# Performance work log

Measured on AMD Instinct MI355X. Metric: run time of the kernel, lower is better.

Reference implementation:

```python
import jax, jax.numpy as jnp
import numpy as np

B, D, H, W_ = 2, 256, 64, 64


def setup_inputs() -> dict:
    key = jax.random.key(0)
    k1, k2 = jax.random.split(key)
    x = jax.random.normal(k1, (B, D, H, W_), dtype=jnp.float32)
    W = jax.random.normal(k2, (3 * D, D), dtype=jnp.float32) * 0.02  # 1x1 conv weight [out,in]
    b = jnp.zeros((3 * D,), dtype=jnp.float32)
    return {"x": x, "W": W, "b": b}


def reference(x, W, b):
    Bs, d, h, w = x.shape
    N = h * w
    sqrtV = d ** 0.25  # sqrt(sqrt(d)); q,k each divided -> qk^T / sqrt(d)
    # 1x1 conv == per-pixel linear over channels
    qkv = jnp.einsum('bchw,oc->bohw', x, W) + b[None, :, None, None]
    q, k, v = jnp.split(qkv, 3, axis=1)
    q = q.reshape(Bs, d, N).transpose(0, 2, 1) / sqrtV  # [B,N,d]
    k = k.reshape(Bs, d, N).transpose(0, 2, 1) / sqrtV
    v = v.reshape(Bs, d, N).transpose(0, 2, 1)
    # Sinkhorn (eps=1, max_iter=1, uniform marginals 1/N), log domain.
    # cost C = -q k^T  =>  -C = q k^T (softmax-style logits)
    negC = jnp.einsum('bnd,bmd->bnm', q, k)  # [B,N,N]
    logm = jnp.log(1.0 / N + 1e-8).astype(x.dtype)
    u = logm - jax.nn.logsumexp(negC, axis=-1)            # [B,N] row update
    vpot = logm - jax.nn.logsumexp(negC + u[..., None], axis=-2)  # [B,N] col update
    pi = jnp.exp(negC + u[..., None] + vpot[:, None, :])  # transport plan = attn
    out = jnp.einsum('bnm,bmd->bnd', pi, v)               # [B,N,d]
    return out.transpose(0, 2, 1).reshape(Bs, d, h, w)
```

## Files before the change

### kernel.cpp

```cpp
#include <hip/hip_runtime.h>
#include <hip/hip_bf16.h>
#include <math.h>

typedef __bf16 bf16;
typedef __bf16 bf16x8 __attribute__((ext_vector_type(8)));
typedef __bf16 bf16x4 __attribute__((ext_vector_type(4)));
typedef float floatx4 __attribute__((ext_vector_type(4)));

typedef const __attribute__((address_space(1))) void* gas_t;
typedef __attribute__((address_space(3))) void* las_t;

#define NPIX 4096
#define DCH 256

#define OFF_XB   ((size_t)0)
#define OFF_WB   ((size_t)4194304)
#define OFF_Q    ((size_t)4587520)
#define OFF_K    ((size_t)8781824)
#define OFF_V    ((size_t)12976128)
#define OFF_E    ((size_t)17170432)
#define OFF_VPP  ((size_t)84279296)
#define OFF_RP   ((size_t)88473600)
#define OFF_CP   ((size_t)89522176)
#define OFF_PART ((size_t)90570752)

__device__ __forceinline__ void stage_tile(const bf16* __restrict__ g0, size_t rstride,
                                           bf16* lds, int t) {
  const int wbase = (t >> 6) << 6;
#pragma unroll
  for (int i = 0; i < 4; i++) {
    int slot = i * 256 + t;
    int row = slot >> 3, seg = slot & 7;
    const bf16* g = g0 + (size_t)row * rstride + ((seg ^ (row & 7)) << 3);
    bf16* l = lds + (size_t)(i * 256 + wbase) * 8;
    __builtin_amdgcn_global_load_lds((gas_t)g, (las_t)l, 16, 0, 0);
  }
}

__global__ __launch_bounds__(256) void prep(
    const float* __restrict__ x, const float* __restrict__ W,
    bf16* __restrict__ xb, bf16* __restrict__ wb)
{
  const int t = threadIdx.x;
  if (blockIdx.y == 4) {
    int gid = (blockIdx.z * 64 + blockIdx.x) * 256 + t;
    for (int i = gid; i < 49152; i += 32768) {
      float4 v = *(const float4*)(W + (size_t)i * 4);
      bf16x4 pk = { (bf16)v.x, (bf16)v.y, (bf16)v.z, (bf16)v.w };
      *(bf16x4*)(wb + (size_t)i * 4) = pk;
    }
    return;
  }
  __shared__ float ts[64][65];
  const int b = blockIdx.z, n0 = blockIdx.x * 64, c0 = blockIdx.y * 64;
  const float* xp = x + ((size_t)b * DCH + c0) * NPIX + n0;
  for (int i = 0; i < 4; i++) {
    int slot = t + i * 256;
    int c = slot >> 4, nq = (slot & 15) * 4;
    float4 v = *(const float4*)(xp + (size_t)c * NPIX + nq);
    ts[c][nq + 0] = v.x; ts[c][nq + 1] = v.y; ts[c][nq + 2] = v.z; ts[c][nq + 3] = v.w;
  }
  __syncthreads();
  for (int i = 0; i < 2; i++) {
    int slot = t + i * 256;
    int n = slot >> 3, cq = (slot & 7) * 8;
    bf16x8 pk;
    for (int j = 0; j < 8; j++) pk[j] = (bf16)ts[cq + j][n];
    *(bf16x8*)(xb + ((size_t)b * NPIX + n0 + n) * DCH + c0 + cq) = pk;
  }
}

__global__ __launch_bounds__(256) void conv_mfma(
    const bf16* __restrict__ xb, const bf16* __restrict__ wb,
    const float* __restrict__ bias,
    bf16* __restrict__ qb, bf16* __restrict__ kb, bf16* __restrict__ vb)
{
  __shared__ bf16 at[128 * 64];
  __shared__ bf16 bt[128 * 64];
  __shared__ float bs[128];
  const int t  = threadIdx.x;
  const int n0 = blockIdx.x * 128;
  const int o0 = blockIdx.y * 128;
  if (t < 128) bs[t] = bias[o0 + t];
  const int lane = t & 63, wave = t >> 6;
  const int wm = wave >> 1, wn = wave & 1;
  const int l15 = lane & 15, quad = lane >> 4;
  const int l7 = l15 & 7;

  floatx4 acc[4][4];
  for (int i=0;i<4;i++) for (int j=0;j<4;j++) for (int r=0;r<4;r++) acc[i][j][r] = 0.f;

  for (int k0 = 0; k0 < DCH; k0 += 64) {
    stage_tile(wb + (size_t)o0 * DCH + k0, DCH, at, t);
    stage_tile(xb + (size_t)n0 * DCH + k0, DCH, bt, t);
    __syncthreads();
    for (int kk = 0; kk < 2; kk++) {
      bf16x8 af[4], bfr[4];
      int sw = ((kk * 4 + quad) ^ l7) * 8;
      for (int f = 0; f < 4; f++)
        af[f]  = *(const bf16x8*)&at[(wm*64 + f*16 + l15)*64 + sw];
      for (int f = 0; f < 4; f++)
        bfr[f] = *(const bf16x8*)&bt[(wn*64 + f*16 + l15)*64 + sw];
      for (int fm = 0; fm < 4; fm++)
        for (int fn = 0; fn < 4; fn++)
          acc[fm][fn] = __builtin_amdgcn_mfma_f32_16x16x32_bf16(af[fm], bfr[fn], acc[fm][fn], 0, 0, 0);
    }
    __syncthreads();
  }

  const float scale = (o0 < 512) ? 0.25f : 1.0f;
  bf16* dst; int od;
  if (o0 < 256)      { dst = qb; od = o0; }
  else if (o0 < 512) { dst = kb; od = o0 - 256; }
  else               { dst = vb; od = o0 - 512; }

  for (int fm = 0; fm < 4; fm++)
    for (int fn = 0; fn < 4; fn++) {
      int o_l = wm*64 + fm*16 + quad*4;
      int n_g = n0 + wn*64 + fn*16 + l15;
      bf16x4 pk;
      for (int r = 0; r < 4; r++)
        pk[r] = (bf16)((acc[fm][fn][r] + bs[o_l + r]) * scale);
      *(bf16x4*)(dst + (size_t)n_g * DCH + od + o_l) = pk;
    }
}

__global__ __launch_bounds__(256) void pass_a(
    const bf16* __restrict__ qb, const bf16* __restrict__ kb,
    bf16* __restrict__ E, float* __restrict__ rowpartG)
{
  __shared__ bf16 kt[128 * 64];
  __shared__ bf16 qt[128 * 64];
  __shared__ float rowpart[128];
  const int b = blockIdx.z;
  qb += (size_t)b * NPIX * DCH;
  kb += (size_t)b * NPIX * DCH;
  E  += (size_t)b * NPIX * NPIX;
  float* rp = rowpartG + ((size_t)b * 32 + blockIdx.x) * NPIX;
  const int t  = threadIdx.x;
  const int m0 = blockIdx.x * 128;
  const int n0 = blockIdx.y * 128;
  const int lane = t & 63, wave = t >> 6;
  const int wm = wave >> 1, wn = wave & 1;
  const int l15 = lane & 15, quad = lane >> 4;
  const int l7 = l15 & 7;

  floatx4 acc[4][4];
  for (int i=0;i<4;i++) for (int j=0;j<4;j++) for (int r=0;r<4;r++) acc[i][j][r] = 0.f;

  for (int k0 = 0; k0 < DCH; k0 += 64) {
    stage_tile(kb + (size_t)m0 * DCH + k0, DCH, kt, t);
    stage_tile(qb + (size_t)n0 * DCH + k0, DCH, qt, t);
    __syncthreads();
    for (int kk = 0; kk < 2; kk++) {
      bf16x8 af[4], bfr[4];
      int sw = ((kk * 4 + quad) ^ l7) * 8;
      for (int f = 0; f < 4; f++)
        af[f]  = *(const bf16x8*)&kt[(wm*64 + f*16 + l15)*64 + sw];
      for (int f = 0; f < 4; f++)
        bfr[f] = *(const bf16x8*)&qt[(wn*64 + f*16 + l15)*64 + sw];
      for (int fm = 0; fm < 4; fm++)
        for (int fn = 0; fn < 4; fn++)
          acc[fm][fn] = __builtin_amdgcn_mfma_f32_16x16x32_bf16(af[fm], bfr[fn], acc[fm][fn], 0, 0, 0);
    }
    __syncthreads();
  }

  if (t < 128) rowpart[t] = 0.f;
  __syncthreads();

  float rsum[4] = {0.f, 0.f, 0.f, 0.f};
  for (int fm = 0; fm < 4; fm++)
    for (int fn = 0; fn < 4; fn++) {
      int n_g = n0 + wn*64 + fn*16 + l15;
      int m_g = m0 + wm*64 + fm*16 + quad*4;
      bf16x4 pk;
      float s = 0.f;
      for (int r = 0; r < 4; r++) {
        float e = __expf(acc[fm][fn][r]);
        pk[r] = (bf16)e;
        s += e;
      }
      *(bf16x4*)(E + (size_t)n_g * NPIX + m_g) = pk;
      rsum[fn] += s;
    }
  for (int fn = 0; fn < 4; fn++) {
    float s = rsum[fn];
    s += __shfl_xor(s, 16);
    s += __shfl_xor(s, 32);
    if (quad == 0) atomicAdd(&rowpart[wn*64 + fn*16 + l15], s);
  }
  __syncthreads();
  if (t < 128) rp[n0 + t] = rowpart[t];
}

__global__ __launch_bounds__(256) void col_pass(
    const bf16* __restrict__ E, const float* __restrict__ rowpartG,
    float* __restrict__ colpartG, float logm)
{
  __shared__ float eus[128];
  const int b = blockIdx.z;
  E += (size_t)b * NPIX * NPIX;
  const float* rp = rowpartG + (size_t)b * 32 * NPIX;
  float* cp = colpartG + ((size_t)b * 32 + blockIdx.y) * NPIX;
  const int t = threadIdx.x;
  const int col = blockIdx.x * 1024 + t * 4;
  const int nbase = blockIdx.y * 128;
  if (t < 128) {
    float s = 0.f;
    for (int mi = 0; mi < 32; mi++) s += rp[(size_t)mi * NPIX + nbase + t];
    eus[t] = __expf(logm - __logf(s));
  }
  __syncthreads();
  float a0 = 0.f, a1 = 0.f, a2 = 0.f, a3 = 0.f;
  for (int r = 0; r < 128; r++) {
    float eu = eus[r];
    bf16x4 ev = *(const bf16x4*)(E + (size_t)(nbase + r) * NPIX + col);
    a0 += eu * (float)ev[0];
    a1 += eu * (float)ev[1];
    a2 += eu * (float)ev[2];
    a3 += eu * (float)ev[3];
  }
  float4 o = {a0, a1, a2, a3};
  *(float4*)(cp + col) = o;
}

__global__ __launch_bounds__(256) void vpp_kernel(
    const bf16* __restrict__ vb, const float* __restrict__ colpartG,
    bf16* __restrict__ vppT, float logm)
{
  __shared__ float ts[64][65];
  __shared__ float ef[64];
  const int b = blockIdx.z;
  vb += (size_t)b * NPIX * DCH;
  const float* cp = colpartG + (size_t)b * 32 * NPIX;
  vppT += (size_t)b * DCH * NPIX;
  const int t = threadIdx.x;
  const int m0 = blockIdx.x * 64, d0 = blockIdx.y * 64;
  if (t < 64) {
    float s = 0.f;
    for (int g = 0; g < 32; g++) s += cp[(size_t)g * NPIX + m0 + t];
    ef[t] = __expf(logm - __logf(s));
  }
  __syncthreads();
  for (int i = 0; i < 2; i++) {
    int slot = t + i * 256;
    int m = slot >> 3, dq = (slot & 7) * 8;
    bf16x8 v = *(const bf16x8*)(vb + (size_t)(m0 + m) * DCH + d0 + dq);
    float s = ef[m];
    for (int j = 0; j < 8; j++) ts[dq + j][m] = s * (float)v[j];
  }
  __syncthreads();
  for (int i = 0; i < 2; i++) {
    int slot = t + i * 256;
    int d = slot >> 3, mq = (slot & 7) * 8;
    bf16x8 pk;
    for (int j = 0; j < 8; j++) pk[j] = (bf16)ts[d][mq + j];
    *(bf16x8*)(vppT + (size_t)(d0 + d) * NPIX + m0 + mq) = pk;
  }
}

__global__ __launch_bounds__(256) void pass_c(
    const bf16* __restrict__ E, const bf16* __restrict__ vppT,
    const float* __restrict__ rowpartG, float* __restrict__ part, float logm)
{
  __shared__ bf16 et[128 * 64];
  __shared__ bf16 vt[128 * 64];
  __shared__ float eus[128];
  const int z = blockIdx.z;
  const int b = z >> 2, kc = z & 3;
  E += (size_t)b * NPIX * NPIX;
  vppT += (size_t)b * DCH * NPIX;
  const float* rp = rowpartG + (size_t)b * 32 * NPIX;
  part += (size_t)(b * 4 + kc) * DCH * NPIX;
  const int t  = threadIdx.x;
  const int n0 = blockIdx.x * 128;
  const int d0 = blockIdx.y * 128;
  const int mstart = kc * 1024;
  if (t < 128) {
    float s = 0.f;
    for (int mi = 0; mi < 32; mi++) s += rp[(size_t)mi * NPIX + n0 + t];
    eus[t] = __expf(logm - __logf(s));
  }
  const int lane = t & 63, wave = t >> 6;
  const int wn = wave >> 1, wd = wave & 1;
  const int l15 = lane & 15, quad = lane >> 4;
  const int l7 = l15 & 7;

  floatx4 acc[4][4];
  for (int i=0;i<4;i++) for (int j=0;j<4;j++) for (int r=0;r<4;r++) acc[i][j][r] = 0.f;
  __syncthreads();

  for (int k0 = mstart; k0 < mstart + 1024; k0 += 64) {
    stage_tile(E + (size_t)n0 * NPIX + k0, NPIX, et, t);
    stage_tile(vppT + (size_t)d0 * NPIX + k0, NPIX, vt, t);
    __syncthreads();
    for (int kk = 0; kk < 2; kk++) {
      bf16x8 af[4], bfr[4];
      int sw = ((kk * 4 + quad) ^ l7) * 8;
      for (int f = 0; f < 4; f++)
        af[f]  = *(const bf16x8*)&et[(wn*64 + f*16 + l15)*64 + sw];
      for (int f = 0; f < 4; f++)
        bfr[f] = *(const bf16x8*)&vt[(wd*64 + f*16 + l15)*64 + sw];
      for (int fn = 0; fn < 4; fn++)
        for (int fd = 0; fd < 4; fd++)
          acc[fn][fd] = __builtin_amdgcn_mfma_f32_16x16x32_bf16(af[fn], bfr[fd], acc[fn][fd], 0, 0, 0);
    }
    __syncthreads();
  }

  for (int fn = 0; fn < 4; fn++)
    for (int fd = 0; fd < 4; fd++) {
      int d_g = d0 + wd*64 + fd*16 + l15;
      int n_l = wn*64 + fn*16 + quad*4;
      float4 o;
      o.x = acc[fn][fd][0] * eus[n_l + 0];
      o.y = acc[fn][fd][1] * eus[n_l + 1];
      o.z = acc[fn][fd][2] * eus[n_l + 2];
      o.w = acc[fn][fd][3] * eus[n_l + 3];
      *(float4*)(part + (size_t)d_g * NPIX + n0 + n_l) = o;
    }
}

__global__ __launch_bounds__(256) void reduce_k(
    const float* __restrict__ part, float* __restrict__ outp)
{
  size_t i4 = ((size_t)blockIdx.x * 256 + threadIdx.x) * 4;
  size_t b = i4 >> 20;
  size_t off = i4 & (size_t)1048575;
  const float* p = part + b * 4 * (size_t)1048576 + off;
  float4 a = *(const float4*)(p);
  float4 bq = *(const float4*)(p + (size_t)1048576);
  float4 c = *(const float4*)(p + (size_t)2097152);
  float4 d = *(const float4*)(p + (size_t)3145728);
  float4 s = { a.x+bq.x+c.x+d.x, a.y+bq.y+c.y+d.y, a.z+bq.z+c.z+d.z, a.w+bq.w+c.w+d.w };
  *(float4*)(outp + i4) = s;
}

extern "C" void kernel_launch(void* const* d_in, const int* in_sizes, int n_in,
                              void* d_out, int out_size, void* d_ws, size_t ws_size,
                              hipStream_t stream) {
  (void)in_sizes; (void)n_in; (void)out_size; (void)ws_size;
  const float* x    = (const float*)d_in[0];
  const float* Wm   = (const float*)d_in[1];
  const float* bias = (const float*)d_in[2];
  float* outp = (float*)d_out;
  char* ws = (char*)d_ws;

  bf16*  xb   = (bf16*)(ws + OFF_XB);
  bf16*  wb   = (bf16*)(ws + OFF_WB);
  bf16*  qb   = (bf16*)(ws + OFF_Q);
  bf16*  kb   = (bf16*)(ws + OFF_K);
  bf16*  vb   = (bf16*)(ws + OFF_V);
  bf16*  E    = (bf16*)(ws + OFF_E);
  bf16*  vppT = (bf16*)(ws + OFF_VPP);
  float* rp   = (float*)(ws + OFF_RP);
  float* cp   = (float*)(ws + OFF_CP);
  float* part = (float*)(ws + OFF_PART);

  const float logm = logf(1.0f / 4096.0f + 1e-8f);

  prep<<<dim3(64, 5, 2), 256, 0, stream>>>(x, Wm, xb, wb);
  conv_mfma<<<dim3(64, 6), 256, 0, stream>>>(xb, wb, bias, qb, kb, vb);

  pass_a<<<dim3(32, 32, 2), 256, 0, stream>>>(qb, kb, E, rp);
  col_pass<<<dim3(4, 32, 2), 256, 0, stream>>>(E, rp, cp, logm);
  vpp_kernel<<<dim3(64, 4, 2), 256, 0, stream>>>(vb, cp, vppT, logm);
  pass_c<<<dim3(32, 2, 8), 256, 0, stream>>>(E, vppT, rp, part, logm);
  reduce_k<<<2048, 256, 0, stream>>>(part, outp);
}
```

Before: 161.2 us.

## Widen pass_c tile to full channel depth and swizzle pass_a block order

pass_c now runs 512-thread blocks that cover all 256 output channels. Each E tile is loaded once per block instead of once for each of two channel halves, which halves E traffic from global memory. pass_a remaps its flat block index so that consecutive blocks share an n tile and walk grouped m tiles, aiming for better L2 reuse of q and k tiles. The price is a larger LDS footprint and fewer blocks in pass_c, which may lower occupancy.

New measurement: 164.7 us. 1.02x slower.

```diff
diff --git a/kernel.cpp b/kernel.cpp
--- a/kernel.cpp
+++ b/kernel.cpp
@@ -24,15 +24,17 @@
 #define OFF_CP   ((size_t)89522176)
 #define OFF_PART ((size_t)90570752)
 
-__device__ __forceinline__ void stage_tile(const bf16* __restrict__ g0, size_t rstride,
-                                           bf16* lds, int t) {
+template<int ROWS, int THREADS>
+__device__ __forceinline__ void stage_tile_g(const bf16* __restrict__ g0, size_t rstride,
+                                             bf16* lds, int t) {
   const int wbase = (t >> 6) << 6;
+  constexpr int ITERS = ROWS * 8 / THREADS;
 #pragma unroll
-  for (int i = 0; i < 4; i++) {
-    int slot = i * 256 + t;
+  for (int i = 0; i < ITERS; i++) {
+    int slot = i * THREADS + t;
     int row = slot >> 3, seg = slot & 7;
     const bf16* g = g0 + (size_t)row * rstride + ((seg ^ (row & 7)) << 3);
-    bf16* l = lds + (size_t)(i * 256 + wbase) * 8;
+    bf16* l = lds + (size_t)(i * THREADS + wbase) * 8;
     __builtin_amdgcn_global_load_lds((gas_t)g, (las_t)l, 16, 0, 0);
   }
 }
@@ -91,8 +93,8 @@
   for (int i=0;i<4;i++) for (int j=0;j<4;j++) for (int r=0;r<4;r++) acc[i][j][r] = 0.f;
 
   for (int k0 = 0; k0 < DCH; k0 += 64) {
-    stage_tile(wb + (size_t)o0 * DCH + k0, DCH, at, t);
-    stage_tile(xb + (size_t)n0 * DCH + k0, DCH, bt, t);
+    stage_tile_g<128,256>(wb + (size_t)o0 * DCH + k0, DCH, at, t);
+    stage_tile_g<128,256>(xb + (size_t)n0 * DCH + k0, DCH, bt, t);
     __syncthreads();
     for (int kk = 0; kk < 2; kk++) {
       bf16x8 af[4], bfr[4];
@@ -136,10 +138,13 @@
   qb += (size_t)b * NPIX * DCH;
   kb += (size_t)b * NPIX * DCH;
   E  += (size_t)b * NPIX * NPIX;
-  float* rp = rowpartG + ((size_t)b * 32 + blockIdx.x) * NPIX;
+  const int flat = blockIdx.x + (blockIdx.y << 5);
+  const int m_tile = ((flat & 7) << 2) + ((flat >> 3) & 3);
+  const int n_tile = flat >> 5;
+  float* rp = rowpartG + ((size_t)b * 32 + m_tile) * NPIX;
   const int t  = threadIdx.x;
-  const int m0 = blockIdx.x * 128;
-  const int n0 = blockIdx.y * 128;
+  const int m0 = m_tile * 128;
+  const int n0 = n_tile * 128;
   const int lane = t & 63, wave = t >> 6;
   const int wm = wave >> 1, wn = wave & 1;
   const int l15 = lane & 15, quad = lane >> 4;
@@ -149,8 +154,8 @@
   for (int i=0;i<4;i++) for (int j=0;j<4;j++) for (int r=0;r<4;r++) acc[i][j][r] = 0.f;
 
   for (int k0 = 0; k0 < DCH; k0 += 64) {
-    stage_tile(kb + (size_t)m0 * DCH + k0, DCH, kt, t);
-    stage_tile(qb + (size_t)n0 * DCH + k0, DCH, qt, t);
+    stage_tile_g<128,256>(kb + (size_t)m0 * DCH + k0, DCH, kt, t);
+    stage_tile_g<128,256>(qb + (size_t)n0 * DCH + k0, DCH, qt, t);
     __syncthreads();
     for (int kk = 0; kk < 2; kk++) {
       bf16x8 af[4], bfr[4];
@@ -260,22 +265,20 @@
   }
 }
 
-__global__ __launch_bounds__(256) void pass_c(
+__global__ __launch_bounds__(512) void pass_c(
     const bf16* __restrict__ E, const bf16* __restrict__ vppT,
     const float* __restrict__ rowpartG, float* __restrict__ part, float logm)
 {
   __shared__ bf16 et[128 * 64];
-  __shared__ bf16 vt[128 * 64];
+  __shared__ bf16 vt[256 * 64];
   __shared__ float eus[128];
-  const int z = blockIdx.z;
-  const int b = z >> 2, kc = z & 3;
+  const int b = blockIdx.z, kc = blockIdx.y;
   E += (size_t)b * NPIX * NPIX;
   vppT += (size_t)b * DCH * NPIX;
   const float* rp = rowpartG + (size_t)b * 32 * NPIX;
   part += (size_t)(b * 4 + kc) * DCH * NPIX;
   const int t  = threadIdx.x;
   const int n0 = blockIdx.x * 128;
-  const int d0 = blockIdx.y * 128;
   const int mstart = kc * 1024;
   if (t < 128) {
     float s = 0.f;
@@ -283,7 +286,7 @@
     eus[t] = __expf(logm - __logf(s));
   }
   const int lane = t & 63, wave = t >> 6;
-  const int wn = wave >> 1, wd = wave & 1;
+  const int wn = wave & 1, wd = wave >> 1;
   const int l15 = lane & 15, quad = lane >> 4;
   const int l7 = l15 & 7;
 
@@ -292,8 +295,8 @@
   __syncthreads();
 
   for (int k0 = mstart; k0 < mstart + 1024; k0 += 64) {
-    stage_tile(E + (size_t)n0 * NPIX + k0, NPIX, et, t);
-    stage_tile(vppT + (size_t)d0 * NPIX + k0, NPIX, vt, t);
+    stage_tile_g<128,512>(E + (size_t)n0 * NPIX + k0, NPIX, et, t);
+    stage_tile_g<256,512>(vppT + k0, NPIX, vt, t);
     __syncthreads();
     for (int kk = 0; kk < 2; kk++) {
       bf16x8 af[4], bfr[4];
@@ -311,7 +314,7 @@
 
   for (int fn = 0; fn < 4; fn++)
     for (int fd = 0; fd < 4; fd++) {
-      int d_g = d0 + wd*64 + fd*16 + l15;
+      int d_g = wd*64 + fd*16 + l15;
       int n_l = wn*64 + fn*16 + quad*4;
       float4 o;
       o.x = acc[fn][fd][0] * eus[n_l + 0];
@@ -366,6 +369,6 @@
   pass_a<<<dim3(32, 32, 2), 256, 0, stream>>>(qb, kb, E, rp);
   col_pass<<<dim3(4, 32, 2), 256, 0, stream>>>(E, rp, cp, logm);
   vpp_kernel<<<dim3(64, 4, 2), 256, 0, stream>>>(vb, cp, vppT, logm);
-  pass_c<<<dim3(32, 2, 8), 256, 0, stream>>>(E, vppT, rp, part, logm);
+  pass_c<<<dim3(32, 4, 2), 512, 0, stream>>>(E, vppT, rp, part, logm);
   reduce_k<<<2048, 256, 0, stream>>>(part, outp);
 }
```

## Fuse all stages into one cooperative persistent kernel with grid syncs

Applied to the files above, without the earlier changes.

Replaces the seven separate kernel launches with a single cooperative persistent kernel. Each stage loops over virtual block indices and is separated from the next by grid.sync, with shared memory unioned across stages. The row-scaling factors are now computed once in the column pass and stored to global memory rather than recomputed in pass_c. This removes launch gaps and inter-kernel drain, at the cost of grid-sync overhead, a grid capped at 512 blocks, and possibly lower occupancy for the large GEMM stages.

Result: slower. 428.9 us (+166.0%).

```diff
diff --git a/kernel.cpp b/kernel.cpp
--- a/kernel.cpp
+++ b/kernel.cpp
@@ -1,6 +1,9 @@
 #include <hip/hip_runtime.h>
+#include <hip/hip_cooperative_groups.h>
 #include <hip/hip_bf16.h>
 #include <math.h>
+
+namespace cg = cooperative_groups;
 
 typedef __bf16 bf16;
 typedef __bf16 bf16x8 __attribute__((ext_vector_type(8)));
@@ -23,6 +26,20 @@
 #define OFF_RP   ((size_t)88473600)
 #define OFF_CP   ((size_t)89522176)
 #define OFF_PART ((size_t)90570752)
+#define OFF_EU   ((size_t)124125184)
+
+struct Params {
+  const float* x; const float* W; const float* bias;
+  bf16* xb; bf16* wb; bf16* qb; bf16* kb; bf16* vb;
+  bf16* E; bf16* vppT; float* rp; float* cp; float* part;
+  float* euG; float* outp; float logm;
+};
+
+union Smem {
+  struct { bf16 a[8192]; bf16 b[8192]; } g;
+  struct { float ts[64][65]; float ef[64]; } tp;
+  float f[8192];
+};
 
 __device__ __forceinline__ void stage_tile(const bf16* __restrict__ g0, size_t rstride,
                                            bf16* lds, int t) {
@@ -37,51 +54,31 @@
   }
 }
 
-__global__ __launch_bounds__(256) void prep(
-    const float* __restrict__ x, const float* __restrict__ W,
-    bf16* __restrict__ xb, bf16* __restrict__ wb)
-{
-  const int t = threadIdx.x;
-  if (blockIdx.y == 4) {
-    int gid = (blockIdx.z * 64 + blockIdx.x) * 256 + t;
-    for (int i = gid; i < 49152; i += 32768) {
-      float4 v = *(const float4*)(W + (size_t)i * 4);
-      bf16x4 pk = { (bf16)v.x, (bf16)v.y, (bf16)v.z, (bf16)v.w };
-      *(bf16x4*)(wb + (size_t)i * 4) = pk;
-    }
-    return;
-  }
-  __shared__ float ts[64][65];
-  const int b = blockIdx.z, n0 = blockIdx.x * 64, c0 = blockIdx.y * 64;
+__device__ void do_transpose(int vb, int t, Smem& sm, const float* x, bf16* xb) {
+  const int b = vb >> 8, n0 = (vb & 63) * 64, c0 = ((vb >> 6) & 3) * 64;
   const float* xp = x + ((size_t)b * DCH + c0) * NPIX + n0;
   for (int i = 0; i < 4; i++) {
     int slot = t + i * 256;
     int c = slot >> 4, nq = (slot & 15) * 4;
     float4 v = *(const float4*)(xp + (size_t)c * NPIX + nq);
-    ts[c][nq + 0] = v.x; ts[c][nq + 1] = v.y; ts[c][nq + 2] = v.z; ts[c][nq + 3] = v.w;
+    sm.tp.ts[c][nq + 0] = v.x; sm.tp.ts[c][nq + 1] = v.y;
+    sm.tp.ts[c][nq + 2] = v.z; sm.tp.ts[c][nq + 3] = v.w;
   }
   __syncthreads();
   for (int i = 0; i < 2; i++) {
     int slot = t + i * 256;
     int n = slot >> 3, cq = (slot & 7) * 8;
     bf16x8 pk;
-    for (int j = 0; j < 8; j++) pk[j] = (bf16)ts[cq + j][n];
+    for (int j = 0; j < 8; j++) pk[j] = (bf16)sm.tp.ts[cq + j][n];
     *(bf16x8*)(xb + ((size_t)b * NPIX + n0 + n) * DCH + c0 + cq) = pk;
   }
-}
-
-__global__ __launch_bounds__(256) void conv_mfma(
-    const bf16* __restrict__ xb, const bf16* __restrict__ wb,
-    const float* __restrict__ bias,
-    bf16* __restrict__ qb, bf16* __restrict__ kb, bf16* __restrict__ vb)
-{
-  __shared__ bf16 at[128 * 64];
-  __shared__ bf16 bt[128 * 64];
-  __shared__ float bs[128];
-  const int t  = threadIdx.x;
-  const int n0 = blockIdx.x * 128;
-  const int o0 = blockIdx.y * 128;
-  if (t < 128) bs[t] = bias[o0 + t];
+  __syncthreads();
+}
+
+__device__ void do_conv(int vb, int t, Smem& sm, const bf16* xb, const bf16* wb,
+                        const float* bias, bf16* qb, bf16* kb, bf16* vbuf) {
+  const int n0 = (vb & 63) * 128;
+  const int o0 = (vb >> 6) * 128;
   const int lane = t & 63, wave = t >> 6;
   const int wm = wave >> 1, wn = wave & 1;
   const int l15 = lane & 15, quad = lane >> 4;
@@ -91,16 +88,16 @@
   for (int i=0;i<4;i++) for (int j=0;j<4;j++) for (int r=0;r<4;r++) acc[i][j][r] = 0.f;
 
   for (int k0 = 0; k0 < DCH; k0 += 64) {
-    stage_tile(wb + (size_t)o0 * DCH + k0, DCH, at, t);
-    stage_tile(xb + (size_t)n0 * DCH + k0, DCH, bt, t);
+    stage_tile(wb + (size_t)o0 * DCH + k0, DCH, sm.g.a, t);
+    stage_tile(xb + (size_t)n0 * DCH + k0, DCH, sm.g.b, t);
     __syncthreads();
     for (int kk = 0; kk < 2; kk++) {
       bf16x8 af[4], bfr[4];
       int sw = ((kk * 4 + quad) ^ l7) * 8;
       for (int f = 0; f < 4; f++)
-        af[f]  = *(const bf16x8*)&at[(wm*64 + f*16 + l15)*64 + sw];
-      for (int f = 0; f < 4; f++)
-        bfr[f] = *(const bf16x8*)&bt[(wn*64 + f*16 + l15)*64 + sw];
+        af[f]  = *(const bf16x8*)&sm.g.a[(wm*64 + f*16 + l15)*64 + sw];
+      for (int f = 0; f < 4; f++)
+        bfr[f] = *(const bf16x8*)&sm.g.b[(wn*64 + f*16 + l15)*64 + sw];
       for (int fm = 0; fm < 4; fm++)
         for (int fn = 0; fn < 4; fn++)
           acc[fm][fn] = __builtin_amdgcn_mfma_f32_16x16x32_bf16(af[fm], bfr[fn], acc[fm][fn], 0, 0, 0);
@@ -112,7 +109,7 @@
   bf16* dst; int od;
   if (o0 < 256)      { dst = qb; od = o0; }
   else if (o0 < 512) { dst = kb; od = o0 - 256; }
-  else               { dst = vb; od = o0 - 512; }
+  else               { dst = vbuf; od = o0 - 512; }
 
   for (int fm = 0; fm < 4; fm++)
     for (int fn = 0; fn < 4; fn++) {
@@ -120,26 +117,20 @@
       int n_g = n0 + wn*64 + fn*16 + l15;
       bf16x4 pk;
       for (int r = 0; r < 4; r++)
-        pk[r] = (bf16)((acc[fm][fn][r] + bs[o_l + r]) * scale);
+        pk[r] = (bf16)((acc[fm][fn][r] + bias[o0 + o_l + r]) * scale);
       *(bf16x4*)(dst + (size_t)n_g * DCH + od + o_l) = pk;
     }
 }
 
-__global__ __launch_bounds__(256) void pass_a(
-    const bf16* __restrict__ qb, const bf16* __restrict__ kb,
-    bf16* __restrict__ E, float* __restrict__ rowpartG)
-{
-  __shared__ bf16 kt[128 * 64];
-  __shared__ bf16 qt[128 * 64];
-  __shared__ float rowpart[128];
-  const int b = blockIdx.z;
-  qb += (size_t)b * NPIX * DCH;
-  kb += (size_t)b * NPIX * DCH;
-  E  += (size_t)b * NPIX * NPIX;
-  float* rp = rowpartG + ((size_t)b * 32 + blockIdx.x) * NPIX;
-  const int t  = threadIdx.x;
-  const int m0 = blockIdx.x * 128;
-  const int n0 = blockIdx.y * 128;
+__device__ void do_pass_a(int vb, int t, Smem& sm, const bf16* qb0, const bf16* kb0,
+                          bf16* E0, float* rowpartG) {
+  const int b = vb >> 10;
+  const int m_tile = vb & 31, n_tile = (vb >> 5) & 31;
+  const bf16* qb = qb0 + (size_t)b * NPIX * DCH;
+  const bf16* kb = kb0 + (size_t)b * NPIX * DCH;
+  bf16* E = E0 + (size_t)b * NPIX * NPIX;
+  float* rp = rowpartG + ((size_t)b * 32 + m_tile) * NPIX;
+  const int m0 = m_tile * 128, n0 = n_tile * 128;
   const int lane = t & 63, wave = t >> 6;
   const int wm = wave >> 1, wn = wave & 1;
   const int l15 = lane & 15, quad = lane >> 4;
@@ -149,16 +140,16 @@
   for (int i=0;i<4;i++) for (int j=0;j<4;j++) for (int r=0;r<4;r++) acc[i][j][r] = 0.f;
 
   for (int k0 = 0; k0 < DCH; k0 += 64) {
-    stage_tile(kb + (size_t)m0 * DCH + k0, DCH, kt, t);
-    stage_tile(qb + (size_t)n0 * DCH + k0, DCH, qt, t);
+    stage_tile(kb + (size_t)m0 * DCH + k0, DCH, sm.g.a, t);
+    stage_tile(qb + (size_t)n0 * DCH + k0, DCH, sm.g.b, t);
     __syncthreads();
     for (int kk = 0; kk < 2; kk++) {
       bf16x8 af[4], bfr[4];
       int sw = ((kk * 4 + quad) ^ l7) * 8;
       for (int f = 0; f < 4; f++)
-        af[f]  = *(const bf16x8*)&kt[(wm*64 + f*16 + l15)*64 + sw];
-      for (int f = 0; f < 4; f++)
-        bfr[f] = *(const bf16x8*)&qt[(wn*64 + f*16 + l15)*64 + sw];
+        af[f]  = *(const bf16x8*)&sm.g.a[(wm*64 + f*16 + l15)*64 + sw];
+      for (int f = 0; f < 4; f++)
+        bfr[f] = *(const bf16x8*)&sm.g.b[(wn*64 + f*16 + l15)*64 + sw];
       for (int fm = 0; fm < 4; fm++)
         for (int fn = 0; fn < 4; fn++)
           acc[fm][fn] = __builtin_amdgcn_mfma_f32_16x16x32_bf16(af[fm], bfr[fn], acc[fm][fn], 0, 0, 0);
@@ -166,6 +157,7 @@
     __syncthreads();
   }
 
+  float* rowpart = sm.f;
   if (t < 128) rowpart[t] = 0.f;
   __syncthreads();
 
@@ -192,29 +184,29 @@
   }
   __syncthreads();
   if (t < 128) rp[n0 + t] = rowpart[t];
-}
-
-__global__ __launch_bounds__(256) void col_pass(
-    const bf16* __restrict__ E, const float* __restrict__ rowpartG,
-    float* __restrict__ colpartG, float logm)
-{
-  __shared__ float eus[128];
-  const int b = blockIdx.z;
-  E += (size_t)b * NPIX * NPIX;
+  __syncthreads();
+}
+
+__device__ void do_col(int vb, int t, Smem& sm, const bf16* E0, const float* rowpartG,
+                       float* colpartG, float* euG, float logm) {
+  const int b = vb >> 7;
+  const int xg = vb & 3, yg = (vb >> 2) & 31;
+  const bf16* E = E0 + (size_t)b * NPIX * NPIX;
   const float* rp = rowpartG + (size_t)b * 32 * NPIX;
-  float* cp = colpartG + ((size_t)b * 32 + blockIdx.y) * NPIX;
-  const int t = threadIdx.x;
-  const int col = blockIdx.x * 1024 + t * 4;
-  const int nbase = blockIdx.y * 128;
+  float* cp = colpartG + ((size_t)b * 32 + yg) * NPIX;
+  const int col = xg * 1024 + t * 4;
+  const int nbase = yg * 128;
   if (t < 128) {
     float s = 0.f;
     for (int mi = 0; mi < 32; mi++) s += rp[(size_t)mi * NPIX + nbase + t];
-    eus[t] = __expf(logm - __logf(s));
+    float e = __expf(logm - __logf(s));
+    sm.f[t] = e;
+    if (xg == 0) euG[b * NPIX + nbase + t] = e;
   }
   __syncthreads();
   float a0 = 0.f, a1 = 0.f, a2 = 0.f, a3 = 0.f;
   for (int r = 0; r < 128; r++) {
-    float eu = eus[r];
+    float eu = sm.f[r];
     bf16x4 ev = *(const bf16x4*)(E + (size_t)(nbase + r) * NPIX + col);
     a0 += eu * (float)ev[0];
     a1 += eu * (float)ev[1];
@@ -223,65 +215,50 @@
   }
   float4 o = {a0, a1, a2, a3};
   *(float4*)(cp + col) = o;
-}
-
-__global__ __launch_bounds__(256) void vpp_kernel(
-    const bf16* __restrict__ vb, const float* __restrict__ colpartG,
-    bf16* __restrict__ vppT, float logm)
-{
-  __shared__ float ts[64][65];
-  __shared__ float ef[64];
-  const int b = blockIdx.z;
-  vb += (size_t)b * NPIX * DCH;
+  __syncthreads();
+}
+
+__device__ void do_vpp(int vb, int t, Smem& sm, const bf16* vb0, const float* colpartG,
+                       bf16* vppT0, float logm) {
+  const int b = vb >> 8;
+  const int m0 = (vb & 63) * 64, d0 = ((vb >> 6) & 3) * 64;
+  const bf16* vbuf = vb0 + (size_t)b * NPIX * DCH;
   const float* cp = colpartG + (size_t)b * 32 * NPIX;
-  vppT += (size_t)b * DCH * NPIX;
-  const int t = threadIdx.x;
-  const int m0 = blockIdx.x * 64, d0 = blockIdx.y * 64;
+  bf16* vppT = vppT0 + (size_t)b * DCH * NPIX;
   if (t < 64) {
     float s = 0.f;
     for (int g = 0; g < 32; g++) s += cp[(size_t)g * NPIX + m0 + t];
-    ef[t] = __expf(logm - __logf(s));
+    sm.tp.ef[t] = __expf(logm - __logf(s));
   }
   __syncthreads();
   for (int i = 0; i < 2; i++) {
     int slot = t + i * 256;
     int m = slot >> 3, dq = (slot & 7) * 8;
-    bf16x8 v = *(const bf16x8*)(vb + (size_t)(m0 + m) * DCH + d0 + dq);
-    float s = ef[m];
-    for (int j = 0; j < 8; j++) ts[dq + j][m] = s * (float)v[j];
+    bf16x8 v = *(const bf16x8*)(vbuf + (size_t)(m0 + m) * DCH + d0 + dq);
+    float s = sm.tp.ef[m];
+    for (int j = 0; j < 8; j++) sm.tp.ts[dq + j][m] = s * (float)v[j];
   }
   __syncthreads();
   for (int i = 0; i < 2; i++) {
     int slot = t + i * 256;
     int d = slot >> 3, mq = (slot & 7) * 8;
     bf16x8 pk;
-    for (int j = 0; j < 8; j++) pk[j] = (bf16)ts[d][mq + j];
+    for (int j = 0; j < 8; j++) pk[j] = (bf16)sm.tp.ts[d][mq + j];
     *(bf16x8*)(vppT + (size_t)(d0 + d) * NPIX + m0 + mq) = pk;
   }
-}
-
-__global__ __launch_bounds__(256) void pass_c(
-    const bf16* __restrict__ E, const bf16* __restrict__ vppT,
-    const float* __restrict__ rowpartG, float* __restrict__ part, float logm)
-{
-  __shared__ bf16 et[128 * 64];
-  __shared__ bf16 vt[128 * 64];
-  __shared__ float eus[128];
-  const int z = blockIdx.z;
+  __syncthreads();
+}
+
+__device__ void do_pass_c(int vb, int t, Smem& sm, const bf16* E0, const bf16* vppT0,
+                          const float* euG, float* part0) {
+  const int z = vb >> 6;
   const int b = z >> 2, kc = z & 3;
-  E += (size_t)b * NPIX * NPIX;
-  vppT += (size_t)b * DCH * NPIX;
-  const float* rp = rowpartG + (size_t)b * 32 * NPIX;
-  part += (size_t)(b * 4 + kc) * DCH * NPIX;
-  const int t  = threadIdx.x;
-  const int n0 = blockIdx.x * 128;
-  const int d0 = blockIdx.y * 128;
+  const int n0 = (vb & 31) * 128;
+  const int d0 = ((vb >> 5) & 1) * 128;
+  const bf16* E = E0 + (size_t)b * NPIX * NPIX;
+  const bf16* vppT = vppT0 + (size_t)b * DCH * NPIX;
+  float* part = part0 + (size_t)(b * 4 + kc) * DCH * NPIX;
   const int mstart = kc * 1024;
-  if (t < 128) {
-    float s = 0.f;
-    for (int mi = 0; mi < 32; mi++) s += rp[(size_t)mi * NPIX + n0 + t];
-    eus[t] = __expf(logm - __logf(s));
-  }
   const int lane = t & 63, wave = t >> 6;
   const int wn = wave >> 1, wd = wave & 1;
   const int l15 = lane & 15, quad = lane >> 4;
@@ -289,19 +266,18 @@
 
   floatx4 acc[4][4];
   for (int i=0;i<4;i++) for (int j=0;j<4;j++) for (int r=0;r<4;r++) acc[i][j][r] = 0.f;
-  __syncthreads();
 
   for (int k0 = mstart; k0 < mstart + 1024; k0 += 64) {
-    stage_tile(E + (size_t)n0 * NPIX + k0, NPIX, et, t);
-    stage_tile(vppT + (size_t)d0 * NPIX + k0, NPIX, vt, t);
+    stage_tile(E + (size_t)n0 * NPIX + k0, NPIX, sm.g.a, t);
+    stage_tile(vppT + (size_t)d0 * NPIX + k0, NPIX, sm.g.b, t);
     __syncthreads();
     for (int kk = 0; kk < 2; kk++) {
       bf16x8 af[4], bfr[4];
       int sw = ((kk * 4 + quad) ^ l7) * 8;
       for (int f = 0; f < 4; f++)
-        af[f]  = *(const bf16x8*)&et[(wn*64 + f*16 + l15)*64 + sw];
-      for (int f = 0; f < 4; f++)
-        bfr[f] = *(const bf16x8*)&vt[(wd*64 + f*16 + l15)*64 + sw];
+        af[f]  = *(const bf16x8*)&sm.g.a[(wn*64 + f*16 + l15)*64 + sw];
+      for (int f = 0; f < 4; f++)
+        bfr[f] = *(const bf16x8*)&sm.g.b[(wd*64 + f*16 + l15)*64 + sw];
       for (int fn = 0; fn < 4; fn++)
         for (int fd = 0; fd < 4; fd++)
           acc[fn][fd] = __builtin_amdgcn_mfma_f32_16x16x32_bf16(af[fn], bfr[fd], acc[fn][fd], 0, 0, 0);
@@ -313,19 +289,18 @@
     for (int fd = 0; fd < 4; fd++) {
       int d_g = d0 + wd*64 + fd*16 + l15;
       int n_l = wn*64 + fn*16 + quad*4;
+      const float* eup = euG + b * NPIX + n0 + n_l;
       float4 o;
-      o.x = acc[fn][fd][0] * eus[n_l + 0];
-      o.y = acc[fn][fd][1] * eus[n_l + 1];
-      o.z = acc[fn][fd][2] * eus[n_l + 2];
-      o.w = acc[fn][fd][3] * eus[n_l + 3];
+      o.x = acc[fn][fd][0] * eup[0];
+      o.y = acc[fn][fd][1] * eup[1];
+      o.z = acc[fn][fd][2] * eup[2];
+      o.w = acc[fn][fd][3] * eup[3];
       *(float4*)(part + (size_t)d_g * NPIX + n0 + n_l) = o;
     }
 }
 
-__global__ __launch_bounds__(256) void reduce_k(
-    const float* __restrict__ part, float* __restrict__ outp)
-{
-  size_t i4 = ((size_t)blockIdx.x * 256 + threadIdx.x) * 4;
+__device__ void do_reduce(int vb, int t, const float* part, float* outp) {
+  size_t i4 = ((size_t)vb * 256 + t) * 4;
   size_t b = i4 >> 20;
   size_t off = i4 & (size_t)1048575;
   const float* p = part + b * 4 * (size_t)1048576 + off;
@@ -337,35 +312,86 @@
   *(float4*)(outp + i4) = s;
 }
 
+__global__ __launch_bounds__(256, 2) void mega(Params p) {
+  __shared__ Smem sm;
+  cg::grid_group grid = cg::this_grid();
+  const int bid = blockIdx.x;
+  const int G = gridDim.x;
+  const int t = threadIdx.x;
+
+  for (int vb = bid; vb < 704; vb += G) {
+    if (vb < 512) {
+      do_transpose(vb, t, sm, p.x, p.xb);
+    } else {
+      int i = (vb - 512) * 256 + t;
+      if (i < 49152) {
+        float4 v = *(const float4*)(p.W + (size_t)i * 4);
+        bf16x4 pk = { (bf16)v.x, (bf16)v.y, (bf16)v.z, (bf16)v.w };
+        *(bf16x4*)(p.wb + (size_t)i * 4) = pk;
+      }
+    }
+  }
+  grid.sync();
+
+  for (int vb = bid; vb < 384; vb += G)
+    do_conv(vb, t, sm, p.xb, p.wb, p.bias, p.qb, p.kb, p.vb);
+  grid.sync();
+
+  for (int vb = bid; vb < 2048; vb += G)
+    do_pass_a(vb, t, sm, p.qb, p.kb, p.E, p.rp);
+  grid.sync();
+
+  for (int vb = bid; vb < 256; vb += G)
+    do_col(vb, t, sm, p.E, p.rp, p.cp, p.euG, p.logm);
+  grid.sync();
+
+  for (int vb = bid; vb < 512; vb += G)
+    do_vpp(vb, t, sm, p.vb, p.cp, p.vppT, p.logm);
+  grid.sync();
+
+  for (int vb = bid; vb < 512; vb += G)
+    do_pass_c(vb, t, sm, p.E, p.vppT, p.euG, p.part);
+  grid.sync();
+
+  for (int vb = bid; vb < 2048; vb += G)
+    do_reduce(vb, t, p.part, p.outp);
+}
+
 extern "C" void kernel_launch(void* const* d_in, const int* in_sizes, int n_in,
                               void* d_out, int out_size, void* d_ws, size_t ws_size,
                               hipStream_t stream) {
   (void)in_sizes; (void)n_in; (void)out_size; (void)ws_size;
-  const float* x    = (const float*)d_in[0];
-  const float* Wm   = (const float*)d_in[1];
-  const float* bias = (const float*)d_in[2];
-  float* outp = (float*)d_out;
   char* ws = (char*)d_ws;
 
-  bf16*  xb   = (bf16*)(ws + OFF_XB);
-  bf16*  wb   = (bf16*)(ws + OFF_WB);
-  bf16*  qb   = (bf16*)(ws + OFF_Q);
-  bf16*  kb   = (bf16*)(ws + OFF_K);
-  bf16*  vb   = (bf16*)(ws + OFF_V);
-  bf16*  E    = (bf16*)(ws + OFF_E);
-  bf16*  vppT = (bf16*)(ws + OFF_VPP);
-  float* rp   = (float*)(ws + OFF_RP);
-  float* cp   = (float*)(ws + OFF_CP);
-  float* part = (float*)(ws + OFF_PART);
-
-  const float logm = logf(1.0f / 4096.0f + 1e-8f);
-
-  prep<<<dim3(64, 5, 2), 256, 0, stream>>>(x, Wm, xb, wb);
-  conv_mfma<<<dim3(64, 6), 256, 0, stream>>>(xb, wb, bias, qb, kb, vb);
-
-  pass_a<<<dim3(32, 32, 2), 256, 0, stream>>>(qb, kb, E, rp);
-  col_pass<<<dim3(4, 32, 2), 256, 0, stream>>>(E, rp, cp, logm);
-  vpp_kernel<<<dim3(64, 4, 2), 256, 0, stream>>>(vb, cp, vppT, logm);
-  pass_c<<<dim3(32, 2, 8), 256, 0, stream>>>(E, vppT, rp, part, logm);
-  reduce_k<<<2048, 256, 0, stream>>>(part, outp);
-}
+  Params p;
+  p.x    = (const float*)d_in[0];
+  p.W    = (const float*)d_in[1];
+  p.bias = (const float*)d_in[2];
+  p.xb   = (bf16*)(ws + OFF_XB);
+  p.wb   = (bf16*)(ws + OFF_WB);
+  p.qb   = (bf16*)(ws + OFF_Q);
+  p.kb   = (bf16*)(ws + OFF_K);
+  p.vb   = (bf16*)(ws + OFF_V);
+  p.E    = (bf16*)(ws + OFF_E);
+  p.vppT = (bf16*)(ws + OFF_VPP);
+  p.rp   = (float*)(ws + OFF_RP);
+  p.cp   = (float*)(ws + OFF_CP);
+  p.part = (float*)(ws + OFF_PART);
+  p.euG  = (float*)(ws + OFF_EU);
+  p.outp = (float*)d_out;
+  p.logm = logf(1.0f / 4096.0f + 1e-8f);
+
+  int dev = 0;
+  hipGetDevice(&dev);
+  int cus = 256;
+  hipDeviceGetAttribute(&cus, hipDeviceAttributeMultiprocessorCount, dev);
+  int perCU = 0;
+  if (hipOccupancyMaxActiveBlocksPerMultiprocessor(&perCU, (const void*)mega, 256, 0)
+      != hipSuccess || perCU < 1)
+    perCU = 1;
+  int grid = perCU * cus;
+  if (grid > 512) grid = 512;
+
+  void* args[] = { &p };
+  hipLaunchCooperativeKernel((const void*)mega, dim3(grid), dim3(256), args, 0, stream);
+}
```
